# Kernel tuning notes

Hardware: AMD Instinct MI355X
Metric: run time of the kernel (lower is better)

The kernel has to match this reference:

```python
import jax, jax.numpy as jnp
import numpy as np

W_CLS, W_BBOX, W_GIOU = 1.0, 5.0, 2.0
EPS = 1e-06


def _cxcywh_to_xyxy(box):
    cx, cy, w, h = box[..., 0], box[..., 1], box[..., 2], box[..., 3]
    return jnp.stack([cx - 0.5 * w, cy - 0.5 * h, cx + 0.5 * w, cy + 0.5 * h], axis=-1)


def _giou(b1, b2):
    # b1: [B, N, 4] xyxy, b2: [B, M, 4] xyxy -> giou [B, N, M]
    area1 = jnp.clip(b1[..., 2] - b1[..., 0], 0) * jnp.clip(b1[..., 3] - b1[..., 1], 0)  # [B,N]
    area2 = jnp.clip(b2[..., 2] - b2[..., 0], 0) * jnp.clip(b2[..., 3] - b2[..., 1], 0)  # [B,M]
    lt = jnp.maximum(b1[:, :, None, :2], b2[:, None, :, :2])  # [B,N,M,2]
    rb = jnp.minimum(b1[:, :, None, 2:], b2[:, None, :, 2:])
    wh = jnp.clip(rb - lt, 0)
    inter = wh[..., 0] * wh[..., 1]
    union = area1[:, :, None] + area2[:, None, :] - inter + EPS
    iou = inter / union
    lt_enc = jnp.minimum(b1[:, :, None, :2], b2[:, None, :, :2])
    rb_enc = jnp.maximum(b1[:, :, None, 2:], b2[:, None, :, 2:])
    wh_enc = jnp.clip(rb_enc - lt_enc, 0)
    enc = wh_enc[..., 0] * wh_enc[..., 1] + EPS
    return iou - (enc - union) / enc


def setup_inputs() -> dict:
    key = jax.random.key(0)
    k1, k2, k3, k4 = jax.random.split(key, 4)
    B, NQ, C, NT = 64, 900, 256, 128
    return {
        "pred_logits": jax.random.normal(k1, (B, NQ, C), dtype=jnp.float32),
        "pred_boxes": jax.random.uniform(k2, (B, NQ, 4), dtype=jnp.float32),
        "tgt_labels": jax.random.randint(k3, (B, NT), 0, C),
        "tgt_boxes": jax.random.uniform(k4, (B, NT, 4), dtype=jnp.float32),
    }


def reference(pred_logits, pred_boxes, tgt_labels, tgt_boxes):
    B, NQ, _ = pred_logits.shape
    NT = tgt_labels.shape[1]
    out_prob = jax.nn.softmax(pred_logits, axis=-1)  # [B,NQ,C]
    # gather class probs at target label ids: [B,NQ,NT]
    idx = jnp.broadcast_to(tgt_labels[:, None, :], (B, NQ, NT))
    cost_cls = -jnp.take_along_axis(out_prob, idx, axis=-1)
    # L1 cdist over cxcywh coords: [B,NQ,NT]
    cost_bbox = jnp.sum(jnp.abs(pred_boxes[:, :, None, :] - tgt_boxes[:, None, :, :]), axis=-1)
    giou = _giou(_cxcywh_to_xyxy(pred_boxes), _cxcywh_to_xyxy(tgt_boxes))
    cost_giou = -giou
    C = W_CLS * cost_cls + W_BBOX * cost_bbox + W_GIOU * cost_giou
    return C
```

## Files before the change

### kernel.cpp

```cpp
#include <hip/hip_runtime.h>

#define BB   64
#define NQ   900
#define NC   256
#define NT   128

#define RPW  4
#define RPB  16
#define CPB  3
#define NBX  19

template<int CTRL>
__device__ __forceinline__ float dpp_add(float x) {
    int y = __builtin_amdgcn_update_dpp(0, __float_as_int(x), CTRL, 0xF, 0xF, true);
    return x + __int_as_float(y);
}

__global__ __launch_bounds__(256) void matcher_kernel(
    const float* __restrict__ logits,
    const float* __restrict__ pboxes,
    const int*   __restrict__ tlabels,
    const float* __restrict__ tboxes,
    float* __restrict__ out)
{
    constexpr float W_BBOX = 5.0f, W_GIOU = 2.0f, EPS = 1e-6f;

    __shared__ float sprob[RPB][NC];
    __shared__ float ssum[RPB];

    const int wave   = threadIdx.x >> 6;
    const int lane   = threadIdx.x & 63;
    const int g      = lane >> 4;
    const int j      = lane & 15;
    const int b      = blockIdx.y;
    const int chunk0 = blockIdx.x * CPB;
    const int wr0    = wave * RPW;

    const int t0 = lane * 2;
    const int2   lbl = *reinterpret_cast<const int2*>(tlabels + b * NT + t0);
    const float4 ta  = *reinterpret_cast<const float4*>(tboxes + ((size_t)b * NT + t0) * 4);
    const float4 tbv = *reinterpret_cast<const float4*>(tboxes + ((size_t)b * NT + t0 + 1) * 4);

    const float ax1 = ta.x - 0.5f * ta.z, ay1 = ta.y - 0.5f * ta.w;
    const float ax2 = ta.x + 0.5f * ta.z, ay2 = ta.y + 0.5f * ta.w;
    const float aarea = fmaxf(ax2 - ax1, 0.0f) * fmaxf(ay2 - ay1, 0.0f);
    const float bx1 = tbv.x - 0.5f * tbv.z, by1 = tbv.y - 0.5f * tbv.w;
    const float bx2 = tbv.x + 0.5f * tbv.z, by2 = tbv.y + 0.5f * tbv.w;
    const float barea = fmaxf(bx2 - bx1, 0.0f) * fmaxf(by2 - by1, 0.0f);

    auto rowptr = [&](int p) {
        int q = (chunk0 + p) * RPB + wr0 + g;
        q = q < NQ - 1 ? q : NQ - 1;
        return logits + ((size_t)b * NQ + q) * NC + j * 4;
    };

    float4 cur[4], nxt[4];
    {
        const float* lp = rowptr(0);
        cur[0] = *reinterpret_cast<const float4*>(lp);
        cur[1] = *reinterpret_cast<const float4*>(lp + 64);
        cur[2] = *reinterpret_cast<const float4*>(lp + 128);
        cur[3] = *reinterpret_cast<const float4*>(lp + 192);
    }

    #pragma unroll
    for (int p = 0; p < CPB; ++p) {
        const int q0 = (chunk0 + p) * RPB + wr0;

        float4 pb[RPW];
        #pragma unroll
        for (int r = 0; r < RPW; ++r) {
            int q = q0 + r; q = q < NQ - 1 ? q : NQ - 1;
            pb[r] = *reinterpret_cast<const float4*>(pboxes + ((size_t)b * NQ + q) * 4);
        }

        if (p + 1 < CPB) {
            const float* lp = rowptr(p + 1);
            nxt[0] = *reinterpret_cast<const float4*>(lp);
            nxt[1] = *reinterpret_cast<const float4*>(lp + 64);
            nxt[2] = *reinterpret_cast<const float4*>(lp + 128);
            nxt[3] = *reinterpret_cast<const float4*>(lp + 192);
        }

        const float e0  = __expf(cur[0].x), e1  = __expf(cur[0].y),
                    e2  = __expf(cur[0].z), e3  = __expf(cur[0].w);
        const float e4  = __expf(cur[1].x), e5  = __expf(cur[1].y),
                    e6  = __expf(cur[1].z), e7  = __expf(cur[1].w);
        const float e8  = __expf(cur[2].x), e9  = __expf(cur[2].y),
                    e10 = __expf(cur[2].z), e11 = __expf(cur[2].w);
        const float e12 = __expf(cur[3].x), e13 = __expf(cur[3].y),
                    e14 = __expf(cur[3].z), e15 = __expf(cur[3].w);

        float* srow = &sprob[wr0 + g][j * 4];
        *reinterpret_cast<float4*>(srow)       = make_float4(e0,  e1,  e2,  e3);
        *reinterpret_cast<float4*>(srow + 64)  = make_float4(e4,  e5,  e6,  e7);
        *reinterpret_cast<float4*>(srow + 128) = make_float4(e8,  e9,  e10, e11);
        *reinterpret_cast<float4*>(srow + 192) = make_float4(e12, e13, e14, e15);

        float s = (((e0 + e1) + (e2 + e3)) + ((e4 + e5) + (e6 + e7)))
                + (((e8 + e9) + (e10 + e11)) + ((e12 + e13) + (e14 + e15)));
        s = dpp_add<0xB1>(s);
        s = dpp_add<0x4E>(s);
        s = dpp_add<0x141>(s);
        s = dpp_add<0x140>(s);
        if (j == 0) ssum[wr0 + g] = s;

        const float4 sums = *reinterpret_cast<const float4*>(&ssum[wr0]);
        const float inv[RPW] = {
            __builtin_amdgcn_rcpf(sums.x), __builtin_amdgcn_rcpf(sums.y),
            __builtin_amdgcn_rcpf(sums.z), __builtin_amdgcn_rcpf(sums.w) };

        #pragma unroll
        for (int r = 0; r < RPW; ++r) {
            const int wr = wr0 + r;
            const float p0 = sprob[wr][lbl.x] * inv[r];
            const float p1 = sprob[wr][lbl.y] * inv[r];

            const float px1 = pb[r].x - 0.5f * pb[r].z, py1 = pb[r].y - 0.5f * pb[r].w;
            const float px2 = pb[r].x + 0.5f * pb[r].z, py2 = pb[r].y + 0.5f * pb[r].w;
            const float parea = fmaxf(px2 - px1, 0.0f) * fmaxf(py2 - py1, 0.0f);

            const float l1a = fabsf(pb[r].x - ta.x) + fabsf(pb[r].y - ta.y)
                            + fabsf(pb[r].z - ta.z) + fabsf(pb[r].w - ta.w);
            const float ia  = fmaxf(fminf(px2, ax2) - fmaxf(px1, ax1), 0.0f)
                            * fmaxf(fminf(py2, ay2) - fmaxf(py1, ay1), 0.0f);
            const float ua  = parea + aarea - ia + EPS;
            const float ea  = fmaxf(fmaxf(px2, ax2) - fminf(px1, ax1), 0.0f)
                            * fmaxf(fmaxf(py2, ay2) - fminf(py1, ay1), 0.0f) + EPS;
            const float gioua = ia * __builtin_amdgcn_rcpf(ua)
                              - (ea - ua) * __builtin_amdgcn_rcpf(ea);
            const float c0 = -p0 + W_BBOX * l1a - W_GIOU * gioua;

            const float l1b = fabsf(pb[r].x - tbv.x) + fabsf(pb[r].y - tbv.y)
                            + fabsf(pb[r].z - tbv.z) + fabsf(pb[r].w - tbv.w);
            const float ib  = fmaxf(fminf(px2, bx2) - fmaxf(px1, bx1), 0.0f)
                            * fmaxf(fminf(py2, by2) - fmaxf(py1, by1), 0.0f);
            const float ub  = parea + barea - ib + EPS;
            const float eb  = fmaxf(fmaxf(px2, bx2) - fminf(px1, bx1), 0.0f)
                            * fmaxf(fmaxf(py2, by2) - fminf(py1, by1), 0.0f) + EPS;
            const float gioub = ib * __builtin_amdgcn_rcpf(ub)
                              - (eb - ub) * __builtin_amdgcn_rcpf(eb);
            const float c1 = -p1 + W_BBOX * l1b - W_GIOU * gioub;

            if (q0 < NQ)
                *reinterpret_cast<float2*>(out + ((size_t)b * NQ + q0 + r) * NT + t0) =
                    make_float2(c0, c1);
        }

        #pragma unroll
        for (int k = 0; k < 4; ++k) cur[k] = nxt[k];
    }
}

extern "C" void kernel_launch(void* const* d_in, const int* in_sizes, int n_in,
                              void* d_out, int out_size, void* d_ws, size_t ws_size,
                              hipStream_t stream) {
    const float* logits  = (const float*)d_in[0];
    const float* pboxes  = (const float*)d_in[1];
    const int*   tlabels = (const int*)d_in[2];
    const float* tboxes  = (const float*)d_in[3];
    float* out = (float*)d_out;

    dim3 grid(NBX, BB);
    matcher_kernel<<<grid, 256, 0, stream>>>(logits, pboxes, tlabels, tboxes, out);
}
```

Before: 22.08 us.

## Stream logits into LDS via async global_load_lds with double buffering

Logit rows are now copied straight from global memory into shared memory with global_load_lds, into two per-wave buffers, and s_waitcnt vmcnt/lgkmcnt is placed by hand so the next chunk's load overlaps the current chunk's compute. The softmax numerator is no longer written back to LDS. The raw logits at the label positions are read and exponentiated again, which drops the LDS store pass and lowers register pressure so occupancy can rise (launch bounds 256,4). The risks are the hand-counted vmcnt values being wrong, which would be a race, and the extra exp per gathered element.

```diff
diff --git a/kernel.cpp b/kernel.cpp
--- a/kernel.cpp
+++ b/kernel.cpp
@@ -10,13 +10,23 @@
 #define CPB  3
 #define NBX  19
 
+typedef const __attribute__((address_space(1))) void gas_t;
+typedef __attribute__((address_space(3))) void las_t;
+
 template<int CTRL>
 __device__ __forceinline__ float dpp_add(float x) {
     int y = __builtin_amdgcn_update_dpp(0, __float_as_int(x), CTRL, 0xF, 0xF, true);
     return x + __int_as_float(y);
 }
 
-__global__ __launch_bounds__(256) void matcher_kernel(
+#define WAITVM(N) do { \
+    asm volatile("s_waitcnt vmcnt(" #N ")" ::: "memory"); \
+    __builtin_amdgcn_sched_barrier(0); } while (0)
+#define WAITLGKM0 do { \
+    asm volatile("s_waitcnt lgkmcnt(0)" ::: "memory"); \
+    __builtin_amdgcn_sched_barrier(0); } while (0)
+
+__global__ __launch_bounds__(256, 4) void matcher_kernel(
     const float* __restrict__ logits,
     const float* __restrict__ pboxes,
     const int*   __restrict__ tlabels,
@@ -25,7 +35,7 @@
 {
     constexpr float W_BBOX = 5.0f, W_GIOU = 2.0f, EPS = 1e-6f;
 
-    __shared__ float sprob[RPB][NC];
+    __shared__ __align__(16) float raw[2][4][RPW * NC];
     __shared__ float ssum[RPB];
 
     const int wave   = threadIdx.x >> 6;
@@ -48,57 +58,47 @@
     const float bx2 = tbv.x + 0.5f * tbv.z, by2 = tbv.y + 0.5f * tbv.w;
     const float barea = fmaxf(bx2 - bx1, 0.0f) * fmaxf(by2 - by1, 0.0f);
 
-    auto rowptr = [&](int p) {
-        int q = (chunk0 + p) * RPB + wr0 + g;
-        q = q < NQ - 1 ? q : NQ - 1;
-        return logits + ((size_t)b * NQ + q) * NC + j * 4;
+    auto stage = [&](int p, int buf) {
+        const int q0 = (chunk0 + p) * RPB + wr0;
+        #pragma unroll
+        for (int k = 0; k < RPW; ++k) {
+            int q = q0 + k; q = q < NQ - 1 ? q : NQ - 1;
+            const float* src = logits + ((size_t)b * NQ + q) * NC + lane * 4;
+            __builtin_amdgcn_global_load_lds((gas_t*)src,
+                                             (las_t*)&raw[buf][wave][k * NC],
+                                             16, 0, 0);
+        }
     };
-
-    float4 cur[4], nxt[4];
-    {
-        const float* lp = rowptr(0);
-        cur[0] = *reinterpret_cast<const float4*>(lp);
-        cur[1] = *reinterpret_cast<const float4*>(lp + 64);
-        cur[2] = *reinterpret_cast<const float4*>(lp + 128);
-        cur[3] = *reinterpret_cast<const float4*>(lp + 192);
-    }
-
-    #pragma unroll
-    for (int p = 0; p < CPB; ++p) {
+    auto loadpb = [&](int p, float4* pbv) {
         const int q0 = (chunk0 + p) * RPB + wr0;
-
-        float4 pb[RPW];
         #pragma unroll
         for (int r = 0; r < RPW; ++r) {
             int q = q0 + r; q = q < NQ - 1 ? q : NQ - 1;
-            pb[r] = *reinterpret_cast<const float4*>(pboxes + ((size_t)b * NQ + q) * 4);
+            pbv[r] = *reinterpret_cast<const float4*>(pboxes + ((size_t)b * NQ + q) * 4);
+        }
+    };
+
+    auto compute = [&](int p, int buf, const float4* pbv) {
+        const int q0 = (chunk0 + p) * RPB + wr0;
+        const float* R = &raw[buf][wave][0];
+
+        float ga[RPW], gb[RPW];
+        #pragma unroll
+        for (int r = 0; r < RPW; ++r) {
+            ga[r] = R[r * NC + lbl.x];
+            gb[r] = R[r * NC + lbl.y];
         }
 
-        if (p + 1 < CPB) {
-            const float* lp = rowptr(p + 1);
-            nxt[0] = *reinterpret_cast<const float4*>(lp);
-            nxt[1] = *reinterpret_cast<const float4*>(lp + 64);
-            nxt[2] = *reinterpret_cast<const float4*>(lp + 128);
-            nxt[3] = *reinterpret_cast<const float4*>(lp + 192);
-        }
+        const float* rr = R + g * NC + j * 4;
+        const float4 v0 = *reinterpret_cast<const float4*>(rr);
+        const float4 v1 = *reinterpret_cast<const float4*>(rr + 64);
+        const float4 v2 = *reinterpret_cast<const float4*>(rr + 128);
+        const float4 v3 = *reinterpret_cast<const float4*>(rr + 192);
 
-        const float e0  = __expf(cur[0].x), e1  = __expf(cur[0].y),
-                    e2  = __expf(cur[0].z), e3  = __expf(cur[0].w);
-        const float e4  = __expf(cur[1].x), e5  = __expf(cur[1].y),
-                    e6  = __expf(cur[1].z), e7  = __expf(cur[1].w);
-        const float e8  = __expf(cur[2].x), e9  = __expf(cur[2].y),
-                    e10 = __expf(cur[2].z), e11 = __expf(cur[2].w);
-        const float e12 = __expf(cur[3].x), e13 = __expf(cur[3].y),
-                    e14 = __expf(cur[3].z), e15 = __expf(cur[3].w);
-
-        float* srow = &sprob[wr0 + g][j * 4];
-        *reinterpret_cast<float4*>(srow)       = make_float4(e0,  e1,  e2,  e3);
-        *reinterpret_cast<float4*>(srow + 64)  = make_float4(e4,  e5,  e6,  e7);
-        *reinterpret_cast<float4*>(srow + 128) = make_float4(e8,  e9,  e10, e11);
-        *reinterpret_cast<float4*>(srow + 192) = make_float4(e12, e13, e14, e15);
-
-        float s = (((e0 + e1) + (e2 + e3)) + ((e4 + e5) + (e6 + e7)))
-                + (((e8 + e9) + (e10 + e11)) + ((e12 + e13) + (e14 + e15)));
+        float s = (((__expf(v0.x) + __expf(v0.y)) + (__expf(v0.z) + __expf(v0.w)))
+                +  ((__expf(v1.x) + __expf(v1.y)) + (__expf(v1.z) + __expf(v1.w))))
+                + (((__expf(v2.x) + __expf(v2.y)) + (__expf(v2.z) + __expf(v2.w)))
+                +  ((__expf(v3.x) + __expf(v3.y)) + (__expf(v3.z) + __expf(v3.w))));
         s = dpp_add<0xB1>(s);
         s = dpp_add<0x4E>(s);
         s = dpp_add<0x141>(s);
@@ -112,16 +112,15 @@
 
         #pragma unroll
         for (int r = 0; r < RPW; ++r) {
-            const int wr = wr0 + r;
-            const float p0 = sprob[wr][lbl.x] * inv[r];
-            const float p1 = sprob[wr][lbl.y] * inv[r];
+            const float p0 = __expf(ga[r]) * inv[r];
+            const float p1 = __expf(gb[r]) * inv[r];
 
-            const float px1 = pb[r].x - 0.5f * pb[r].z, py1 = pb[r].y - 0.5f * pb[r].w;
-            const float px2 = pb[r].x + 0.5f * pb[r].z, py2 = pb[r].y + 0.5f * pb[r].w;
+            const float px1 = pbv[r].x - 0.5f * pbv[r].z, py1 = pbv[r].y - 0.5f * pbv[r].w;
+            const float px2 = pbv[r].x + 0.5f * pbv[r].z, py2 = pbv[r].y + 0.5f * pbv[r].w;
             const float parea = fmaxf(px2 - px1, 0.0f) * fmaxf(py2 - py1, 0.0f);
 
-            const float l1a = fabsf(pb[r].x - ta.x) + fabsf(pb[r].y - ta.y)
-                            + fabsf(pb[r].z - ta.z) + fabsf(pb[r].w - ta.w);
+            const float l1a = fabsf(pbv[r].x - ta.x) + fabsf(pbv[r].y - ta.y)
+                            + fabsf(pbv[r].z - ta.z) + fabsf(pbv[r].w - ta.w);
             const float ia  = fmaxf(fminf(px2, ax2) - fmaxf(px1, ax1), 0.0f)
                             * fmaxf(fminf(py2, ay2) - fmaxf(py1, ay1), 0.0f);
             const float ua  = parea + aarea - ia + EPS;
@@ -131,8 +130,8 @@
                               - (ea - ua) * __builtin_amdgcn_rcpf(ea);
             const float c0 = -p0 + W_BBOX * l1a - W_GIOU * gioua;
 
-            const float l1b = fabsf(pb[r].x - tbv.x) + fabsf(pb[r].y - tbv.y)
-                            + fabsf(pb[r].z - tbv.z) + fabsf(pb[r].w - tbv.w);
+            const float l1b = fabsf(pbv[r].x - tbv.x) + fabsf(pbv[r].y - tbv.y)
+                            + fabsf(pbv[r].z - tbv.z) + fabsf(pbv[r].w - tbv.w);
             const float ib  = fmaxf(fminf(px2, bx2) - fmaxf(px1, bx1), 0.0f)
                             * fmaxf(fminf(py2, by2) - fmaxf(py1, by1), 0.0f);
             const float ub  = parea + barea - ib + EPS;
@@ -146,10 +145,27 @@
                 *reinterpret_cast<float2*>(out + ((size_t)b * NQ + q0 + r) * NT + t0) =
                     make_float2(c0, c1);
         }
+    };
 
-        #pragma unroll
-        for (int k = 0; k < 4; ++k) cur[k] = nxt[k];
-    }
+    float4 pb0[RPW], pb1[RPW];
+
+    stage(0, 0);
+    loadpb(0, pb0);
+    stage(1, 1);
+    loadpb(1, pb1);
+
+    WAITVM(8);
+    compute(0, 0, pb0);
+
+    WAITLGKM0;
+    stage(2, 0);
+    loadpb(2, pb0);
+
+    WAITVM(8);
+    compute(1, 1, pb1);
+
+    WAITVM(0);
+    compute(2, 0, pb0);
 }
 
 extern "C" void kernel_launch(void* const* d_in, const int* in_sizes, int n_in,
```

After: 24.78 us. 1.12x slower.
